# Performance work log

Hardware: AMD Instinct MI355X
Metric: run time of the kernel (lower is better)

## Reference

```python
import jax, jax.numpy as jnp
import numpy as np

B, L, DIM, N, D = 8, 273, 1536, 12, 128
ZS, F_HIS = 256, 32  # image tokens per frame, cache_frame_max
EPS = 1e-6


def rmsnorm(x, g, eps=EPS):
    return x * jax.lax.rsqrt(jnp.mean(x * x, axis=-1, keepdims=True) + eps) * g


def rope_apply(x, freqs):
    # x: [B, T, N, D]; freqs: [T, D//2] angles. Rotate consecutive pairs.
    xp = x.reshape(*x.shape[:-1], D // 2, 2)
    c = jnp.cos(freqs)[None, :, None, :]
    s = jnp.sin(freqs)[None, :, None, :]
    o1 = xp[..., 0] * c - xp[..., 1] * s
    o2 = xp[..., 0] * s + xp[..., 1] * c
    return jnp.stack([o1, o2], axis=-1).reshape(x.shape)


def setup_inputs() -> dict:
    key = jax.random.key(0)
    ks = jax.random.split(key, 10)
    rn = lambda k, shp, sc=1.0: jax.random.normal(k, shp, dtype=jnp.float32) * sc
    return {
        "x": rn(ks[0], (B, L, DIM)),
        "w_q": rn(ks[1], (DIM, DIM), 0.02), "b_q": jnp.zeros((DIM,), jnp.float32),
        "w_k": rn(ks[2], (DIM, DIM), 0.02), "b_k": jnp.zeros((DIM,), jnp.float32),
        "w_v": rn(ks[3], (DIM, DIM), 0.02), "b_v": jnp.zeros((DIM,), jnp.float32),
        "w_o": rn(ks[4], (DIM, DIM), 0.02), "b_o": jnp.zeros((DIM,), jnp.float32),
        "g_q": jnp.ones((DIM,), jnp.float32), "g_k": jnp.ones((DIM,), jnp.float32),
        "cache_k": rn(ks[5], (B, F_HIS * L, N, D)),
        "cache_v": rn(ks[6], (B, F_HIS * L, N, D)),
        "rope_table": jax.random.uniform(ks[7], (64, L, D // 2), dtype=jnp.float32) * (2.0 * np.pi),
        "read_rope_indices": jnp.arange(F_HIS, dtype=jnp.int32),
        "current_frame_idx": 20,
    }


def reference(x, w_q, b_q, w_k, b_k, w_v, b_v, w_o, b_o, g_q, g_k,
              cache_k, cache_v, rope_table, read_rope_indices, current_frame_idx):
    b, s = x.shape[:2]
    f = 1  # one new frame per step (s == L)
    # qkv projections with RMSNorm over full dim (pre head split)
    q = rmsnorm(x @ w_q.T + b_q, g_q).reshape(b, s, N, D)
    k = rmsnorm(x @ w_k.T + b_k, g_k).reshape(b, s, N, D)
    v = (x @ w_v.T + b_v).reshape(b, s, N, D)
    # KV-cache ring-buffer store at slot = frame_idx % cache_frame_max
    slot = current_frame_idx % F_HIS
    cache_k = jax.lax.dynamic_update_slice(cache_k, k, (0, slot * L, 0, 0))
    cache_v = jax.lax.dynamic_update_slice(cache_v, v, (0, slot * L, 0, 0))
    # RoPE angles: history for each cache slot, last for the current frame
    freqs_his = rope_table[read_rope_indices].reshape(F_HIS * L, D // 2)
    freqs_last = rope_table[current_frame_idx]  # [L, D//2]
    q_r = rope_apply(q, freqs_last)
    k_r = rope_apply(cache_k, freqs_his)
    # frame-major views: [b, frames, tokens_per_frame, n, d]
    q_r = q_r.reshape(b, f, L, N, D)
    k_r = k_r.reshape(b, F_HIS, L, N, D)
    v_his = cache_v.reshape(b, F_HIS, L, N, D)
    q_img, k_img, v_img = q_r[:, :, :ZS], k_r[:, :, :ZS], v_his[:, :, :ZS]
    # temporal attention per spatial (image) token, non-causal, masked to valid frames
    scale = 1.0 / jnp.sqrt(jnp.asarray(D, jnp.float32))
    scores = jnp.einsum('bfznd,bgznd->bznfg', q_img, k_img) * scale  # [b,zs,n,f,f_his]
    valid = jnp.minimum(current_frame_idx + 1, F_HIS)
    keep = jnp.arange(F_HIS) < valid
    scores = jnp.where(keep[None, None, None, None, :], scores, -1e30)
    p = jax.nn.softmax(scores, axis=-1)
    x_img = jnp.einsum('bznfg,bgznd->bfznd', p, v_img)  # [b, f, zs, n, d]
    # condition tokens bypass attention: pass through v of the current frame
    v_cond = v.reshape(b, f, L, N, D)[:, :, ZS:]
    out = jnp.concatenate([x_img, v_cond], axis=2).reshape(b, s, N * D)
    return out @ w_o.T + b_o


if __name__ == '__main__':
    o = reference(**setup_inputs())
    print(o.shape)
```

## Files before the change

kernel.cpp:

```cpp
#include <hip/hip_runtime.h>
#include <hip/hip_bf16.h>
#include <stdint.h>

typedef unsigned short u16;
typedef __attribute__((ext_vector_type(8))) short bf16x8;
typedef __attribute__((ext_vector_type(4))) float f32x4;

#define B_    8
#define L_    273
#define DIM_  1536
#define NH_   12
#define DH_   128
#define ZS_   256
#define FH_   32
#define MROWS (B_ * L_)
#define MPAD  2304
#define NQKV  4608

#define OFF_XB    0ULL
#define OFF_WB    7077888ULL
#define OFF_WOB   21233664ULL
#define OFF_BQKV  25952256ULL
#define OFF_CQKV  25970688ULL
#define OFF_ATTN  68438016ULL

__device__ __forceinline__ u16 f2bf(float f) {
  __hip_bfloat16 h = __float2bfloat16(f);
  return *reinterpret_cast<u16*>(&h);
}

__device__ __forceinline__ void gload_lds16(const u16* g, u16* l) {
  __builtin_amdgcn_global_load_lds(
      (const __attribute__((address_space(1))) void*)g,
      (__attribute__((address_space(3))) void*)l,
      16, 0, 0);
}

__global__ void cast_pad_kernel(const float* __restrict__ src, u16* __restrict__ dst,
                                int n_src, int n_tot) {
  int i = blockIdx.x * 256 + threadIdx.x;
  if (i >= n_tot) return;
  float v = (i < n_src) ? src[i] : 0.f;
  dst[i] = f2bf(v);
}

__global__ void pack_bias_kernel(const float* __restrict__ bq, const float* __restrict__ bk,
                                 const float* __restrict__ bv, float* __restrict__ dst) {
  int i = blockIdx.x * 256 + threadIdx.x;
  if (i >= NQKV) return;
  float v;
  if (i < DIM_)            v = bq[i];
  else if (i < 2 * DIM_)   v = bk[i - DIM_];
  else                     v = bv[i - 2 * DIM_];
  dst[i] = v;
}

__global__ __launch_bounds__(256)
void gemm_bt_kernel(const u16* __restrict__ A, const u16* __restrict__ Bm,
                    const float* __restrict__ bias, float* __restrict__ C,
                    int K, int ldc, int Mvalid) {
  const int tn = blockIdx.x, tm = blockIdx.y;
  const int tid = threadIdx.x;
  const int lane = tid & 63;
  const int wid = tid >> 6;
  const int wm = wid >> 1, wn = wid & 1;

  __shared__ __align__(16) u16 As[128 * 32];
  __shared__ __align__(16) u16 Bs[128 * 32];

  f32x4 acc[4][4] = {};

  const int srow = tid >> 2;
  const int scol = (tid & 3) * 8;
  const u16* Abase = A + (size_t)(tm * 128 + srow) * K + scol;
  const u16* Bbase = Bm + (size_t)(tn * 128 + srow) * K + scol;
  u16* lAs = &As[srow * 32 + scol];
  u16* lBs = &Bs[srow * 32 + scol];
  const size_t rstep = (size_t)64 * K;

  const int ko = (lane >> 4) * 8;
  const int rA = wm * 64 + (lane & 15);
  const int rB = wn * 64 + (lane & 15);

  for (int kt = 0; kt < K; kt += 32) {
    __syncthreads();
    gload_lds16(Abase + kt,         lAs);
    gload_lds16(Abase + kt + rstep, lAs + 64 * 32);
    gload_lds16(Bbase + kt,         lBs);
    gload_lds16(Bbase + kt + rstep, lBs + 64 * 32);
    __syncthreads();

    bf16x8 af[4], bfr[4];
#pragma unroll
    for (int f = 0; f < 4; ++f) {
      af[f]  = *(const bf16x8*)&As[(rA + f * 16) * 32 + ko];
      bfr[f] = *(const bf16x8*)&Bs[(rB + f * 16) * 32 + ko];
    }
#pragma unroll
    for (int fm = 0; fm < 4; ++fm)
#pragma unroll
      for (int fn = 0; fn < 4; ++fn)
        acc[fm][fn] = __builtin_amdgcn_mfma_f32_16x16x32_bf16(af[fm], bfr[fn], acc[fm][fn], 0, 0, 0);
  }

  const int m0 = tm * 128 + wm * 64 + (lane >> 4) * 4;
  const int n0 = tn * 128 + wn * 64 + (lane & 15);
#pragma unroll
  for (int fm = 0; fm < 4; ++fm) {
#pragma unroll
    for (int fn = 0; fn < 4; ++fn) {
      const int n = n0 + fn * 16;
      const float bv = bias[n];
#pragma unroll
      for (int r = 0; r < 4; ++r) {
        const int m = m0 + fm * 16 + r;
        if (m < Mvalid) C[(size_t)m * ldc + n] = acc[fm][fn][r] + bv;
      }
    }
  }
}

__global__ __launch_bounds__(256)
void rmsnorm_rope_kernel(float* __restrict__ C, const float* __restrict__ g_q,
                         const float* __restrict__ g_k, const float* __restrict__ rope_table,
                         const int* __restrict__ cf_ptr) {
  const int m = blockIdx.x;
  const int l = m % L_;
  const int tid = threadIdx.x;
  const int cf = *cf_ptr;
  float* row = C + (size_t)m * NQKV;
  __shared__ float red[4];

  for (int sec = 0; sec < 2; ++sec) {
    float* p = row + sec * DIM_;
    const float* gw = sec ? g_k : g_q;
    float2 v[3];
    float ss = 0.f;
#pragma unroll
    for (int j = 0; j < 3; ++j) {
      int pj = tid + j * 256;
      v[j] = *(const float2*)&p[pj * 2];
      ss += v[j].x * v[j].x + v[j].y * v[j].y;
    }
#pragma unroll
    for (int o = 32; o; o >>= 1) ss += __shfl_xor(ss, o);
    if ((tid & 63) == 0) red[tid >> 6] = ss;
    __syncthreads();
    const float tot = red[0] + red[1] + red[2] + red[3];
    const float r = rsqrtf(tot * (1.f / DIM_) + 1e-6f);
#pragma unroll
    for (int j = 0; j < 3; ++j) {
      int pj = tid + j * 256;
      float y0 = v[j].x * r * gw[pj * 2];
      float y1 = v[j].y * r * gw[pj * 2 + 1];
      if (sec == 0) {
        float fr = rope_table[((size_t)cf * L_ + l) * 64 + (pj & 63)];
        float sn, cn;
        __sincosf(fr, &sn, &cn);
        float o0 = y0 * cn - y1 * sn;
        float o1 = y0 * sn + y1 * cn;
        y0 = o0; y1 = o1;
      }
      *(float2*)&p[pj * 2] = make_float2(y0, y1);
    }
    __syncthreads();
  }
}

__global__ __launch_bounds__(256)
void attention_kernel(const float* __restrict__ C, const float* __restrict__ cache_k,
                      const float* __restrict__ cache_v, const float* __restrict__ rope_table,
                      const int* __restrict__ rope_idx, const int* __restrict__ cf_ptr,
                      u16* __restrict__ attn_in) {
  const int w = blockIdx.x * 4 + (threadIdx.x >> 6);
  const int lane = threadIdx.x & 63;
  const int n = w % NH_;
  const int z = (w / NH_) & (ZS_ - 1);
  const int b = w / (NH_ * ZS_);
  const int cf = *cf_ptr;
  const int slot = cf % FH_;
  const int valid = min(cf + 1, FH_);
  const int d0 = lane * 2;

  const size_t crow = (size_t)(b * L_ + z) * NQKV + n * DH_ + d0;
  const float2 q = *(const float2*)&C[crow];

  float mx = -1e30f, lsum = 0.f, a0 = 0.f, a1 = 0.f;
  for (int g = 0; g < valid; ++g) {
    const int fi = rope_idx[g];
    const float fr = rope_table[((size_t)fi * L_ + z) * 64 + lane];
    float sn, cn;
    __sincosf(fr, &sn, &cn);
    const size_t coff = ((((size_t)b * FH_ + g) * L_ + z) * NH_ + n) * DH_ + d0;
    const float2 kv = (g == slot) ? *(const float2*)&C[crow + DIM_]
                                  : *(const float2*)&cache_k[coff];
    const float kr0 = kv.x * cn - kv.y * sn;
    const float kr1 = kv.x * sn + kv.y * cn;
    float part = q.x * kr0 + q.y * kr1;
#pragma unroll
    for (int o = 32; o; o >>= 1) part += __shfl_xor(part, o);
    const float score = part * 0.088388347648318447f;
    const float nm = fmaxf(mx, score);
    const float scl = __expf(mx - nm);
    const float pw = __expf(score - nm);
    const float2 vv = (g == slot) ? *(const float2*)&C[crow + 2 * DIM_]
                                  : *(const float2*)&cache_v[coff];
    lsum = lsum * scl + pw;
    a0 = a0 * scl + pw * vv.x;
    a1 = a1 * scl + pw * vv.y;
    mx = nm;
  }
  const float inv = 1.f / lsum;
  const uint32_t packed = (uint32_t)f2bf(a0 * inv) | ((uint32_t)f2bf(a1 * inv) << 16);
  *(uint32_t*)&attn_in[(size_t)(b * L_ + z) * DIM_ + n * DH_ + d0] = packed;
}

__global__ void vcond_kernel(const float* __restrict__ C, u16* __restrict__ attn_in) {
  int i = blockIdx.x * 256 + threadIdx.x;
  const int total = B_ * (L_ - ZS_) * DIM_;
  if (i >= total) return;
  int col = i % DIM_;
  int r = i / DIM_;
  int b = r / (L_ - ZS_);
  int lz = r % (L_ - ZS_);
  int mrow = b * L_ + ZS_ + lz;
  attn_in[(size_t)mrow * DIM_ + col] = f2bf(C[(size_t)mrow * NQKV + 2 * DIM_ + col]);
}

extern "C" void kernel_launch(void* const* d_in, const int* in_sizes, int n_in,
                              void* d_out, int out_size, void* d_ws, size_t ws_size,
                              hipStream_t stream) {
  const float* x       = (const float*)d_in[0];
  const float* w_q     = (const float*)d_in[1];
  const float* b_q     = (const float*)d_in[2];
  const float* w_k     = (const float*)d_in[3];
  const float* b_k     = (const float*)d_in[4];
  const float* w_v     = (const float*)d_in[5];
  const float* b_v     = (const float*)d_in[6];
  const float* w_o     = (const float*)d_in[7];
  const float* b_o     = (const float*)d_in[8];
  const float* g_q     = (const float*)d_in[9];
  const float* g_k     = (const float*)d_in[10];
  const float* cache_k = (const float*)d_in[11];
  const float* cache_v = (const float*)d_in[12];
  const float* rope_tb = (const float*)d_in[13];
  const int*   rope_ix = (const int*)d_in[14];
  const int*   cf      = (const int*)d_in[15];

  char* ws = (char*)d_ws;
  u16*   xb      = (u16*)(ws + OFF_XB);
  u16*   wb      = (u16*)(ws + OFF_WB);
  u16*   wob     = (u16*)(ws + OFF_WOB);
  float* bqkv    = (float*)(ws + OFF_BQKV);
  float* Cq      = (float*)(ws + OFF_CQKV);
  u16*   attn_in = (u16*)(ws + OFF_ATTN);

  const int WN = DIM_ * DIM_;

  cast_pad_kernel<<<(MPAD * DIM_ + 255) / 256, 256, 0, stream>>>(x, xb, MROWS * DIM_, MPAD * DIM_);
  cast_pad_kernel<<<(WN + 255) / 256, 256, 0, stream>>>(w_q, wb,           WN, WN);
  cast_pad_kernel<<<(WN + 255) / 256, 256, 0, stream>>>(w_k, wb + WN,      WN, WN);
  cast_pad_kernel<<<(WN + 255) / 256, 256, 0, stream>>>(w_v, wb + 2 * WN,  WN, WN);
  cast_pad_kernel<<<(WN + 255) / 256, 256, 0, stream>>>(w_o, wob,          WN, WN);
  pack_bias_kernel<<<(NQKV + 255) / 256, 256, 0, stream>>>(b_q, b_k, b_v, bqkv);

  gemm_bt_kernel<<<dim3(NQKV / 128, MPAD / 128), 256, 0, stream>>>(xb, wb, bqkv, Cq, DIM_, NQKV, MPAD);

  rmsnorm_rope_kernel<<<MROWS, 256, 0, stream>>>(Cq, g_q, g_k, rope_tb, cf);

  attention_kernel<<<(B_ * ZS_ * NH_) / 4, 256, 0, stream>>>(Cq, cache_k, cache_v, rope_tb, rope_ix, cf, attn_in);

  vcond_kernel<<<(B_ * (L_ - ZS_) * DIM_ + 255) / 256, 256, 0, stream>>>(Cq, attn_in);

  gemm_bt_kernel<<<dim3(DIM_ / 128, MPAD / 128), 256, 0, stream>>>(attn_in, wob, b_o, (float*)d_out, DIM_, DIM_, MROWS);
}
```

Baseline: 260.7 us.

## Store QKV in bf16, precompute rope sincos, vectorize casts and attention loads

The QKV GEMM now writes bf16 output instead of fp32, which halves the intermediate traffic for the rmsnorm, attention and vcond kernels. Rmsnorm/rope now runs only on the 256 image-token rows, since condition tokens need only v. A separate kernel precomputes the sin/cos for cache-key rope once per frame and token, so attention no longer recomputes it for every batch and head. The cast kernels and attention use wider vector loads, with each wave handling two heads at four elements per lane. Rounding q, k and v to bf16 before normalization and attention adds precision error.

```diff
diff --git a/kernel.cpp b/kernel.cpp
--- a/kernel.cpp
+++ b/kernel.cpp
@@ -22,11 +22,16 @@
 #define OFF_WOB   21233664ULL
 #define OFF_BQKV  25952256ULL
 #define OFF_CQKV  25970688ULL
-#define OFF_ATTN  68438016ULL
+#define OFF_ATTN  47204352ULL
+#define OFF_SC    54282240ULL
 
 __device__ __forceinline__ u16 f2bf(float f) {
   __hip_bfloat16 h = __float2bfloat16(f);
   return *reinterpret_cast<u16*>(&h);
+}
+__device__ __forceinline__ float bf2f(u16 v) {
+  uint32_t u = ((uint32_t)v) << 16;
+  return __uint_as_float(u);
 }
 
 __device__ __forceinline__ void gload_lds16(const u16* g, u16* l) {
@@ -36,12 +41,22 @@
       16, 0, 0);
 }
 
-__global__ void cast_pad_kernel(const float* __restrict__ src, u16* __restrict__ dst,
-                                int n_src, int n_tot) {
+__global__ void cast_pad8_kernel(const float* __restrict__ src, u16* __restrict__ dst,
+                                 int n_src8, int n_tot8) {
   int i = blockIdx.x * 256 + threadIdx.x;
-  if (i >= n_tot) return;
-  float v = (i < n_src) ? src[i] : 0.f;
-  dst[i] = f2bf(v);
+  if (i >= n_tot8) return;
+  uint4 o;
+  if (i < n_src8) {
+    const float4 a = ((const float4*)src)[i * 2];
+    const float4 b = ((const float4*)src)[i * 2 + 1];
+    o.x = (uint32_t)f2bf(a.x) | ((uint32_t)f2bf(a.y) << 16);
+    o.y = (uint32_t)f2bf(a.z) | ((uint32_t)f2bf(a.w) << 16);
+    o.z = (uint32_t)f2bf(b.x) | ((uint32_t)f2bf(b.y) << 16);
+    o.w = (uint32_t)f2bf(b.z) | ((uint32_t)f2bf(b.w) << 16);
+  } else {
+    o = make_uint4(0, 0, 0, 0);
+  }
+  ((uint4*)dst)[i] = o;
 }
 
 __global__ void pack_bias_kernel(const float* __restrict__ bq, const float* __restrict__ bk,
@@ -56,9 +71,22 @@
 }
 
 __global__ __launch_bounds__(256)
+void sincos_kernel(const float* __restrict__ rope_table, const int* __restrict__ rope_idx,
+                   float* __restrict__ sctab) {
+  const int idx = blockIdx.x * 4 + (threadIdx.x >> 6);
+  const int j = threadIdx.x & 63;
+  const int f = idx / ZS_, z = idx % ZS_;
+  const int fi = rope_idx[f];
+  const float fr = rope_table[((size_t)fi * L_ + z) * 64 + j];
+  float sn, cn;
+  __sincosf(fr, &sn, &cn);
+  *(float2*)&sctab[((size_t)idx << 7) + 2 * j] = make_float2(sn, cn);
+}
+
+__global__ __launch_bounds__(256)
 void gemm_bt_kernel(const u16* __restrict__ A, const u16* __restrict__ Bm,
-                    const float* __restrict__ bias, float* __restrict__ C,
-                    int K, int ldc, int Mvalid) {
+                    const float* __restrict__ bias, void* __restrict__ Cv,
+                    int K, int ldc, int Mvalid, int bf16out) {
   const int tn = blockIdx.x, tm = blockIdx.y;
   const int tid = threadIdx.x;
   const int lane = tid & 63;
@@ -114,33 +142,40 @@
 #pragma unroll
       for (int r = 0; r < 4; ++r) {
         const int m = m0 + fm * 16 + r;
-        if (m < Mvalid) C[(size_t)m * ldc + n] = acc[fm][fn][r] + bv;
+        if (m < Mvalid) {
+          const float val = acc[fm][fn][r] + bv;
+          if (bf16out) ((u16*)Cv)[(size_t)m * ldc + n] = f2bf(val);
+          else         ((float*)Cv)[(size_t)m * ldc + n] = val;
+        }
       }
     }
   }
 }
 
 __global__ __launch_bounds__(256)
-void rmsnorm_rope_kernel(float* __restrict__ C, const float* __restrict__ g_q,
+void rmsnorm_rope_kernel(u16* __restrict__ C, const float* __restrict__ g_q,
                          const float* __restrict__ g_k, const float* __restrict__ rope_table,
                          const int* __restrict__ cf_ptr) {
-  const int m = blockIdx.x;
-  const int l = m % L_;
+  const int z = blockIdx.x % ZS_;
+  const int b = blockIdx.x / ZS_;
+  const int m = b * L_ + z;
   const int tid = threadIdx.x;
   const int cf = *cf_ptr;
-  float* row = C + (size_t)m * NQKV;
+  u16* row = C + (size_t)m * NQKV;
   __shared__ float red[4];
 
   for (int sec = 0; sec < 2; ++sec) {
-    float* p = row + sec * DIM_;
+    u16* p = row + sec * DIM_;
     const float* gw = sec ? g_k : g_q;
-    float2 v[3];
+    float vx[3], vy[3];
     float ss = 0.f;
 #pragma unroll
     for (int j = 0; j < 3; ++j) {
       int pj = tid + j * 256;
-      v[j] = *(const float2*)&p[pj * 2];
-      ss += v[j].x * v[j].x + v[j].y * v[j].y;
+      uint32_t u = *(const uint32_t*)&p[pj * 2];
+      vx[j] = bf2f((u16)(u & 0xffff));
+      vy[j] = bf2f((u16)(u >> 16));
+      ss += vx[j] * vx[j] + vy[j] * vy[j];
     }
 #pragma unroll
     for (int o = 32; o; o >>= 1) ss += __shfl_xor(ss, o);
@@ -151,80 +186,98 @@
 #pragma unroll
     for (int j = 0; j < 3; ++j) {
       int pj = tid + j * 256;
-      float y0 = v[j].x * r * gw[pj * 2];
-      float y1 = v[j].y * r * gw[pj * 2 + 1];
+      float y0 = vx[j] * r * gw[pj * 2];
+      float y1 = vy[j] * r * gw[pj * 2 + 1];
       if (sec == 0) {
-        float fr = rope_table[((size_t)cf * L_ + l) * 64 + (pj & 63)];
+        float fr = rope_table[((size_t)cf * L_ + z) * 64 + (pj & 63)];
         float sn, cn;
         __sincosf(fr, &sn, &cn);
         float o0 = y0 * cn - y1 * sn;
         float o1 = y0 * sn + y1 * cn;
         y0 = o0; y1 = o1;
       }
-      *(float2*)&p[pj * 2] = make_float2(y0, y1);
+      *(uint32_t*)&p[pj * 2] = (uint32_t)f2bf(y0) | ((uint32_t)f2bf(y1) << 16);
     }
     __syncthreads();
   }
 }
 
 __global__ __launch_bounds__(256)
-void attention_kernel(const float* __restrict__ C, const float* __restrict__ cache_k,
-                      const float* __restrict__ cache_v, const float* __restrict__ rope_table,
-                      const int* __restrict__ rope_idx, const int* __restrict__ cf_ptr,
-                      u16* __restrict__ attn_in) {
+void attention_kernel(const u16* __restrict__ Cq, const float* __restrict__ cache_k,
+                      const float* __restrict__ cache_v, const float* __restrict__ sctab,
+                      const int* __restrict__ cf_ptr, u16* __restrict__ attn_in) {
   const int w = blockIdx.x * 4 + (threadIdx.x >> 6);
   const int lane = threadIdx.x & 63;
-  const int n = w % NH_;
-  const int z = (w / NH_) & (ZS_ - 1);
-  const int b = w / (NH_ * ZS_);
+  const int hp = w % 6;
+  const int z = (w / 6) % ZS_;
+  const int b = w / (6 * ZS_);
+  const int h = lane >> 5, il = lane & 31;
+  const int n = hp * 2 + h;
+  const int d0 = il * 4;
   const int cf = *cf_ptr;
   const int slot = cf % FH_;
   const int valid = min(cf + 1, FH_);
-  const int d0 = lane * 2;
 
   const size_t crow = (size_t)(b * L_ + z) * NQKV + n * DH_ + d0;
-  const float2 q = *(const float2*)&C[crow];
-
-  float mx = -1e30f, lsum = 0.f, a0 = 0.f, a1 = 0.f;
+  float q0, q1, q2, q3;
+  {
+    ushort4 qv = *(const ushort4*)&Cq[crow];
+    q0 = bf2f(qv.x); q1 = bf2f(qv.y); q2 = bf2f(qv.z); q3 = bf2f(qv.w);
+  }
+
+  float mx = -1e30f, lsum = 0.f;
+  float a0 = 0.f, a1 = 0.f, a2 = 0.f, a3 = 0.f;
   for (int g = 0; g < valid; ++g) {
-    const int fi = rope_idx[g];
-    const float fr = rope_table[((size_t)fi * L_ + z) * 64 + lane];
-    float sn, cn;
-    __sincosf(fr, &sn, &cn);
-    const size_t coff = ((((size_t)b * FH_ + g) * L_ + z) * NH_ + n) * DH_ + d0;
-    const float2 kv = (g == slot) ? *(const float2*)&C[crow + DIM_]
-                                  : *(const float2*)&cache_k[coff];
-    const float kr0 = kv.x * cn - kv.y * sn;
-    const float kr1 = kv.x * sn + kv.y * cn;
-    float part = q.x * kr0 + q.y * kr1;
-#pragma unroll
-    for (int o = 32; o; o >>= 1) part += __shfl_xor(part, o);
+    const float4 sc = *(const float4*)&sctab[((size_t)(g * ZS_ + z) << 7) + d0];
+    float k0, k1, k2, k3, v0, v1, v2, v3;
+    if (g == slot) {
+      ushort4 kv = *(const ushort4*)&Cq[crow + DIM_];
+      ushort4 vv = *(const ushort4*)&Cq[crow + 2 * DIM_];
+      k0 = bf2f(kv.x); k1 = bf2f(kv.y); k2 = bf2f(kv.z); k3 = bf2f(kv.w);
+      v0 = bf2f(vv.x); v1 = bf2f(vv.y); v2 = bf2f(vv.z); v3 = bf2f(vv.w);
+    } else {
+      const size_t coff = ((((size_t)b * FH_ + g) * L_ + z) * NH_ + n) * DH_ + d0;
+      const float4 kk = *(const float4*)&cache_k[coff];
+      const float4 vv = *(const float4*)&cache_v[coff];
+      k0 = kk.x; k1 = kk.y; k2 = kk.z; k3 = kk.w;
+      v0 = vv.x; v1 = vv.y; v2 = vv.z; v3 = vv.w;
+    }
+    const float kr0 = k0 * sc.y - k1 * sc.x;
+    const float kr1 = k0 * sc.x + k1 * sc.y;
+    const float kr2 = k2 * sc.w - k3 * sc.z;
+    const float kr3 = k2 * sc.z + k3 * sc.w;
+    float part = q0 * kr0 + q1 * kr1 + q2 * kr2 + q3 * kr3;
+#pragma unroll
+    for (int o = 16; o; o >>= 1) part += __shfl_xor(part, o);
     const float score = part * 0.088388347648318447f;
     const float nm = fmaxf(mx, score);
     const float scl = __expf(mx - nm);
     const float pw = __expf(score - nm);
-    const float2 vv = (g == slot) ? *(const float2*)&C[crow + 2 * DIM_]
-                                  : *(const float2*)&cache_v[coff];
     lsum = lsum * scl + pw;
-    a0 = a0 * scl + pw * vv.x;
-    a1 = a1 * scl + pw * vv.y;
+    a0 = a0 * scl + pw * v0;
+    a1 = a1 * scl + pw * v1;
+    a2 = a2 * scl + pw * v2;
+    a3 = a3 * scl + pw * v3;
     mx = nm;
   }
   const float inv = 1.f / lsum;
-  const uint32_t packed = (uint32_t)f2bf(a0 * inv) | ((uint32_t)f2bf(a1 * inv) << 16);
-  *(uint32_t*)&attn_in[(size_t)(b * L_ + z) * DIM_ + n * DH_ + d0] = packed;
-}
-
-__global__ void vcond_kernel(const float* __restrict__ C, u16* __restrict__ attn_in) {
+  uint2 o;
+  o.x = (uint32_t)f2bf(a0 * inv) | ((uint32_t)f2bf(a1 * inv) << 16);
+  o.y = (uint32_t)f2bf(a2 * inv) | ((uint32_t)f2bf(a3 * inv) << 16);
+  *(uint2*)&attn_in[(size_t)(b * L_ + z) * DIM_ + n * DH_ + d0] = o;
+}
+
+__global__ void vcond_kernel(const u16* __restrict__ Cq, u16* __restrict__ attn_in) {
   int i = blockIdx.x * 256 + threadIdx.x;
-  const int total = B_ * (L_ - ZS_) * DIM_;
-  if (i >= total) return;
-  int col = i % DIM_;
-  int r = i / DIM_;
+  const int tot = B_ * (L_ - ZS_) * DIM_ / 8;
+  if (i >= tot) return;
+  int e = i * 8;
+  int col = e % DIM_;
+  int r = e / DIM_;
   int b = r / (L_ - ZS_);
   int lz = r % (L_ - ZS_);
-  int mrow = b * L_ + ZS_ + lz;
-  attn_in[(size_t)mrow * DIM_ + col] = f2bf(C[(size_t)mrow * NQKV + 2 * DIM_ + col]);
+  size_t mrow = (size_t)b * L_ + ZS_ + lz;
+  *(uint4*)&attn_in[mrow * DIM_ + col] = *(const uint4*)&Cq[mrow * NQKV + 2 * DIM_ + col];
 }
 
 extern "C" void kernel_launch(void* const* d_in, const int* in_sizes, int n_in,
@@ -252,25 +305,30 @@
   u16*   wb      = (u16*)(ws + OFF_WB);
   u16*   wob     = (u16*)(ws + OFF_WOB);
   float* bqkv    = (float*)(ws + OFF_BQKV);
-  float* Cq      = (float*)(ws + OFF_CQKV);
+  u16*   Cq      = (u16*)(ws + OFF_CQKV);
   u16*   attn_in = (u16*)(ws + OFF_ATTN);
+  float* sctab   = (float*)(ws + OFF_SC);
 
   const int WN = DIM_ * DIM_;
-
-  cast_pad_kernel<<<(MPAD * DIM_ + 255) / 256, 256, 0, stream>>>(x, xb, MROWS * DIM_, MPAD * DIM_);
-  cast_pad_kernel<<<(WN + 255) / 256, 256, 0, stream>>>(w_q, wb,           WN, WN);
-  cast_pad_kernel<<<(WN + 255) / 256, 256, 0, stream>>>(w_k, wb + WN,      WN, WN);
-  cast_pad_kernel<<<(WN + 255) / 256, 256, 0, stream>>>(w_v, wb + 2 * WN,  WN, WN);
-  cast_pad_kernel<<<(WN + 255) / 256, 256, 0, stream>>>(w_o, wob,          WN, WN);
+  const int WN8 = WN / 8;
+  const int X8 = MROWS * DIM_ / 8;
+  const int XT8 = MPAD * DIM_ / 8;
+
+  cast_pad8_kernel<<<(XT8 + 255) / 256, 256, 0, stream>>>(x, xb, X8, XT8);
+  cast_pad8_kernel<<<(WN8 + 255) / 256, 256, 0, stream>>>(w_q, wb,          WN8, WN8);
+  cast_pad8_kernel<<<(WN8 + 255) / 256, 256, 0, stream>>>(w_k, wb + WN,     WN8, WN8);
+  cast_pad8_kernel<<<(WN8 + 255) / 256, 256, 0, stream>>>(w_v, wb + 2 * WN, WN8, WN8);
+  cast_pad8_kernel<<<(WN8 + 255) / 256, 256, 0, stream>>>(w_o, wob,         WN8, WN8);
   pack_bias_kernel<<<(NQKV + 255) / 256, 256, 0, stream>>>(b_q, b_k, b_v, bqkv);
-
-  gemm_bt_kernel<<<dim3(NQKV / 128, MPAD / 128), 256, 0, stream>>>(xb, wb, bqkv, Cq, DIM_, NQKV, MPAD);
-
-  rmsnorm_rope_kernel<<<MROWS, 256, 0, stream>>>(Cq, g_q, g_k, rope_tb, cf);
-
-  attention_kernel<<<(B_ * ZS_ * NH_) / 4, 256, 0, stream>>>(Cq, cache_k, cache_v, rope_tb, rope_ix, cf, attn_in);
-
-  vcond_kernel<<<(B_ * (L_ - ZS_) * DIM_ + 255) / 256, 256, 0, stream>>>(Cq, attn_in);
-
-  gemm_bt_kernel<<<dim3(DIM_ / 128, MPAD / 128), 256, 0, stream>>>(attn_in, wob, b_o, (float*)d_out, DIM_, DIM_, MROWS);
-}
+  sincos_kernel<<<FH_ * ZS_ / 4, 256, 0, stream>>>(rope_tb, rope_ix, sctab);
+
+  gemm_bt_kernel<<<dim3(NQKV / 128, MPAD / 128), 256, 0, stream>>>(xb, wb, bqkv, Cq, DIM_, NQKV, MPAD, 1);
+
+  rmsnorm_rope_kernel<<<B_ * ZS_, 256, 0, stream>>>(Cq, g_q, g_k, rope_tb, cf);
+
+  attention_kernel<<<(B_ * ZS_ * 6) / 4, 256, 0, stream>>>(Cq, cache_k, cache_v, sctab, cf, attn_in);
+
+  vcond_kernel<<<(B_ * (L_ - ZS_) * DIM_ / 8 + 255) / 256, 256, 0, stream>>>(Cq, attn_in);
+
+  gemm_bt_kernel<<<dim3(DIM_ / 128, MPAD / 128), 256, 0, stream>>>(attn_in, wob, b_o, (float*)d_out, DIM_, DIM_, MROWS, 0);
+}
```

After: 250.1 us. -4.1%, faster.
